# Kernel tuning notes

Measured on AMD Instinct MI355X. Metric: run time of the kernel, lower is better.

## Reference

```python
import jax, jax.numpy as jnp
import numpy as np

K_ORDER = 3
GRID_N = 10
GRID_LO, GRID_HI = -2.0, 2.0
LAYERS = [(49, 256), (256, 256), (256, 10)]
NCOEF = GRID_N + K_ORDER  # 13


def mish(x):
    return x * jnp.tanh(jax.nn.softplus(x))


def bspline_basis(x):
    # x: (B, in) -> basis (B, in, GRID_N + K_ORDER)
    h = (GRID_HI - GRID_LO) / GRID_N
    knots = GRID_LO + h * jnp.arange(-K_ORDER, GRID_N + K_ORDER + 1, dtype=x.dtype)  # (G+2k+1,)
    xx = x[..., None]
    B = ((xx >= knots[:-1]) & (xx < knots[1:])).astype(x.dtype)  # degree-0, (B,in,G+2k)
    for d in range(1, K_ORDER + 1):
        left = (xx - knots[: -(d + 1)]) / (knots[d:-1] - knots[: -(d + 1)]) * B[..., :-1]
        right = (knots[d + 1:] - xx) / (knots[d + 1:] - knots[1:-d]) * B[..., 1:]
        B = left + right
    return B  # (B, in, G+k)


def kan_layer(x, coef, scale_base, scale_sp, bias):
    # x: (B,in); coef: (in,out,G+k); scales: (in,out); bias: (out,)
    basis = bspline_basis(x)                                   # (B,in,G+k)
    spline = jnp.einsum('big,iog->bo', basis, coef * scale_sp[..., None])
    base = jnp.einsum('bi,io->bo', mish(x), scale_base)
    return base + spline + bias


def setup_inputs() -> dict:
    key = jax.random.key(0)
    ks = jax.random.split(key, 1 + 4 * len(LAYERS))
    inp = {'x': jax.random.normal(ks[0], (8192, 1, 28, 28), dtype=jnp.float32)}
    i = 1
    for li, (fin, fout) in enumerate(LAYERS, start=1):
        inp[f'coef{li}'] = 0.1 * jax.random.normal(ks[i], (fin, fout, NCOEF), dtype=jnp.float32); i += 1
        inp[f'sb{li}'] = 1.0 + 0.1 * jax.random.normal(ks[i], (fin, fout), dtype=jnp.float32); i += 1
        inp[f'sp{li}'] = 1.0 + 0.1 * jax.random.normal(ks[i], (fin, fout), dtype=jnp.float32); i += 1
        inp[f'b{li}'] = jnp.zeros((fout,), dtype=jnp.float32); i += 1
    return inp


def reference(x, coef1, sb1, sp1, b1, coef2, sb2, sp2, b2, coef3, sb3, sp3, b3):
    B = x.shape[0]
    # avg_pool2d(x, 4): 28x28 -> 7x7
    h = x.reshape(B, 1, 7, 4, 7, 4).mean(axis=(3, 5))
    h = h.reshape(B, 49)
    h = kan_layer(h, coef1, sb1, sp1, b1)
    h = kan_layer(h, coef2, sb2, sp2, b2)
    h = kan_layer(h, coef3, sb3, sp3, b3)
    return jax.nn.log_softmax(h, axis=1)
```

## Files before the change

kernel.cpp:

```cpp
#include <hip/hip_runtime.h>
#include <hip/hip_bf16.h>

typedef __bf16 bf16x8_t __attribute__((ext_vector_type(8)));
typedef float f32x4_t __attribute__((ext_vector_type(4)));
using bf16 = __hip_bfloat16;

#define ASG __attribute__((address_space(1)))
#define ASL __attribute__((address_space(3)))

__device__ __forceinline__ void gld_lds16(const void* g, void* l) {
  __builtin_amdgcn_global_load_lds((ASG void*)const_cast<void*>(g),
                                   (ASL void*)l, 16, 0, 0);
}

__device__ __forceinline__ unsigned short f2bf_bits(float v) {
  __hip_bfloat16 h = __float2bfloat16(v);
  return *reinterpret_cast<unsigned short*>(&h);
}

__device__ __forceinline__ float mish_f(float x) {
  float z = __expf(x);
  float n = z * (z + 2.0f);
  float m = x * n / (n + 2.0f);
  return (x > 10.0f) ? x : m;
}

__device__ __forceinline__ void kan_feats28(bf16* dst, float x) {
  unsigned int* d32 = (unsigned int*)dst;
#pragma unroll
  for (int d = 0; d < 7; ++d) d32[d] = 0u;
  float t = (x + 3.2f) * 2.5f;
  if (t >= 0.0f && t < 16.0f) {
    float tf = floorf(t);
    int c = (int)tf;
    float u = t - tf;
    float um = 1.0f - u;
    float u2 = u * u, u3 = u2 * u;
    const float s6 = 1.0f / 6.0f;
    float w0 = um * um * um * s6;
    float w1 = (3.0f * u3 - 6.0f * u2 + 4.0f) * s6;
    float w2 = (-3.0f * u3 + 3.0f * u2 + 3.0f * u + 1.0f) * s6;
    float w3 = u3 * s6;
    int j0 = c - 3;
    if (j0 >= 0)               dst[j0]     = __float2bfloat16(w0);
    if (j0 >= -1 && j0 <= 11)  dst[j0 + 1] = __float2bfloat16(w1);
    if (j0 >= -2 && j0 <= 10)  dst[j0 + 2] = __float2bfloat16(w2);
    if (j0 <= 9)               dst[j0 + 3] = __float2bfloat16(w3);
  }
  dst[13] = __float2bfloat16(mish_f(x));
}

__global__ __launch_bounds__(256) void prep_all(
    const float* __restrict__ c1, const float* __restrict__ sb1, const float* __restrict__ sp1,
    const float* __restrict__ c2, const float* __restrict__ sb2, const float* __restrict__ sp2,
    const float* __restrict__ c3, const float* __restrict__ sb3, const float* __restrict__ sp3,
    bf16* __restrict__ W1t, bf16* __restrict__ W2f, bf16* __restrict__ W3f) {
  const int b = blockIdx.x, o = threadIdx.x;
  float vals[14];
  if (b < 49) {
    const int i = b;
    const size_t io = (size_t)i * 256 + o;
    const float spv = sp1[io];
#pragma unroll
    for (int r = 0; r < 13; ++r) vals[r] = c1[io * 13 + r] * spv;
    vals[13] = sb1[io];
    unsigned int* dst = (unsigned int*)(W1t + (size_t)o * 704 + i * 14);
#pragma unroll
    for (int d = 0; d < 7; ++d)
      dst[d] = (unsigned int)f2bf_bits(vals[2 * d]) |
               ((unsigned int)f2bf_bits(vals[2 * d + 1]) << 16);
  } else if (b == 49) {
    unsigned int* dst = (unsigned int*)(W1t + (size_t)o * 704 + 686);
#pragma unroll
    for (int d = 0; d < 9; ++d) dst[d] = 0u;
  } else if (b < 306) {
    const int i = b - 50;
    const size_t io = (size_t)i * 256 + o;
    const float spv = sp2[io];
#pragma unroll
    for (int r = 0; r < 13; ++r) vals[r] = c2[io * 13 + r] * spv;
    vals[13] = sb2[io];
    const int ntg = o >> 4, lr = o & 15;
#pragma unroll
    for (int d = 0; d < 7; ++d) {
      const int k2 = i * 14 + 2 * d;
      const int kc = k2 / 224, rem = k2 % 224;
      const int ks = rem / 32, r2 = rem % 32, quad = r2 / 8, el = r2 % 8;
      const size_t off = ((size_t)((kc * 7 + ks) * 16 + ntg)) * 512 + lr * 32 + quad * 8 + el;
      *(unsigned int*)(W2f + off) = (unsigned int)f2bf_bits(vals[2 * d]) |
                                    ((unsigned int)f2bf_bits(vals[2 * d + 1]) << 16);
    }
  } else {
    const int i = b - 306;
    if (o < 10) {
      const size_t io = (size_t)i * 10 + o;
      const float spv = sp3[io];
#pragma unroll
      for (int r = 0; r < 13; ++r) vals[r] = c3[io * 13 + r] * spv;
      vals[13] = sb3[io];
#pragma unroll
      for (int d = 0; d < 7; ++d) {
        const int k2 = i * 14 + 2 * d;
        const int s = k2 >> 5, r2 = k2 & 31;
        const size_t off = (size_t)s * 512 + o * 32 + (r2 >> 3) * 8 + (r2 & 7);
        *(unsigned int*)(W3f + off) = (unsigned int)f2bf_bits(vals[2 * d]) |
                                      ((unsigned int)f2bf_bits(vals[2 * d + 1]) << 16);
      }
    } else if (o < 16) {
#pragma unroll
      for (int d = 0; d < 7; ++d) {
        const int k2 = i * 14 + 2 * d;
        const int s = k2 >> 5, r2 = k2 & 31;
        *(unsigned int*)(W3f + (size_t)s * 512 + o * 32 + (r2 >> 3) * 8 + (r2 & 7)) = 0u;
      }
    }
  }
}

__global__ __launch_bounds__(256) void pool_basis1(const float* __restrict__ x,
                                                   bf16* __restrict__ A1) {
  __shared__ __align__(16) float xs[3136];
  __shared__ __align__(16) bf16 arow[4 * 704];
  const int b4 = blockIdx.x * 4, t = threadIdx.x;
  const float4* xsrc = (const float4*)(x + (size_t)b4 * 784);
  float4* xd = (float4*)xs;
#pragma unroll
  for (int l = t; l < 784; l += 256) xd[l] = xsrc[l];
  __syncthreads();
  if (t < 196) {
    const int img = t / 49, p = t - img * 49;
    const int oh = p / 7, ow = p - oh * 7;
    const float* xi = xs + img * 784;
    float s = 0.f;
#pragma unroll
    for (int r = 0; r < 4; ++r)
#pragma unroll
      for (int c = 0; c < 4; ++c) s += xi[(oh * 4 + r) * 28 + ow * 4 + c];
    kan_feats28(&arow[img * 704 + p * 14], s * (1.0f / 16.0f));
  } else if (t < 232) {
    const int q = t - 196;
    const int img = q / 9, d = q - img * 9;
    ((unsigned int*)(arow + img * 704 + 686))[d] = 0u;
  }
  __syncthreads();
  uint4* dst = (uint4*)(A1 + (size_t)b4 * 704);
  const uint4* src = (const uint4*)arow;
#pragma unroll
  for (int l = t; l < 352; l += 256) dst[l] = src[l];
}

__global__ __launch_bounds__(256) void gemm1s(
    const bf16* __restrict__ A, const bf16* __restrict__ Wt,
    const float* __restrict__ bias, float* __restrict__ H) {
  constexpr int K = 704;
  __shared__ __align__(16) bf16 As[64 * 64];
  __shared__ __align__(16) bf16 Bs[64 * 64];
  const int t = threadIdx.x;
  const int wv = t >> 6, lane = t & 63, quad = lane >> 4, lr = lane & 15;
  const int n0 = blockIdx.x * 64;
  const int m0 = blockIdx.y * 64;
  const int srow0 = lane >> 3;
  const int cg = (lane & 7) ^ srow0;
  const bf16* gA0 = A + (size_t)(m0 + 8 * wv + srow0) * K + cg * 8;
  const bf16* gA1 = A + (size_t)(m0 + 32 + 8 * wv + srow0) * K + cg * 8;
  const bf16* gB0 = Wt + (size_t)(n0 + 8 * wv + srow0) * K + cg * 8;
  const bf16* gB1 = Wt + (size_t)(n0 + 32 + 8 * wv + srow0) * K + cg * 8;
  char* const lA = (char*)As + wv * 1024;
  char* const lB = (char*)Bs + wv * 1024;
  const int wm = (wv & 1) * 32, wn = (wv >> 1) * 32;
  const int swz = lr & 7;
  f32x4_t acc00 = {0.f, 0.f, 0.f, 0.f}, acc01 = acc00, acc10 = acc00, acc11 = acc00;
  for (int k0 = 0; k0 < K; k0 += 64) {
    gld_lds16(gA0 + k0, lA);
    gld_lds16(gA1 + k0, lA + 4096);
    gld_lds16(gB0 + k0, lB);
    gld_lds16(gB1 + k0, lB + 4096);
    __syncthreads();
#pragma unroll
    for (int s = 0; s < 2; ++s) {
      const int co = ((s * 4 + quad) ^ swz) * 16;
      bf16x8_t a0 = *(const bf16x8_t*)((char*)As + (wm + lr) * 128 + co);
      bf16x8_t a1 = *(const bf16x8_t*)((char*)As + (wm + 16 + lr) * 128 + co);
      bf16x8_t b0 = *(const bf16x8_t*)((char*)Bs + (wn + lr) * 128 + co);
      bf16x8_t b1 = *(const bf16x8_t*)((char*)Bs + (wn + 16 + lr) * 128 + co);
      acc00 = __builtin_amdgcn_mfma_f32_16x16x32_bf16(a0, b0, acc00, 0, 0, 0);
      acc01 = __builtin_amdgcn_mfma_f32_16x16x32_bf16(a0, b1, acc01, 0, 0, 0);
      acc10 = __builtin_amdgcn_mfma_f32_16x16x32_bf16(a1, b0, acc10, 0, 0, 0);
      acc11 = __builtin_amdgcn_mfma_f32_16x16x32_bf16(a1, b1, acc11, 0, 0, 0);
    }
    __syncthreads();
  }
  const int cb = n0 + wn + lr;
  const float bn0 = bias[cb], bn1 = bias[cb + 16];
#pragma unroll
  for (int r = 0; r < 4; ++r) {
    const size_t row = (size_t)(m0 + wm + quad * 4 + r);
    H[row * 256 + cb] = acc00[r] + bn0;
    H[row * 256 + cb + 16] = acc01[r] + bn1;
    H[(row + 16) * 256 + cb] = acc10[r] + bn0;
    H[(row + 16) * 256 + cb + 16] = acc11[r] + bn1;
  }
}

__global__ __launch_bounds__(512, 4) void kan_gemm2(
    const float* __restrict__ Hin, const bf16* __restrict__ W2f,
    float* __restrict__ Hp) {
  __shared__ __align__(16) bf16 As[2][64 * 232];
  const int t = threadIdx.x;
  const int w = t >> 6, lane = t & 63, quad = lane >> 4, lr = lane & 15;
  const int m0 = blockIdx.x * 64;
  const int z = blockIdx.y;
  const int ej = t & 15, er0 = (t >> 4) & 31;
  const int foff = lr * 32 + quad * 8;
  f32x4_t acc[4][2];
#pragma unroll
  for (int m = 0; m < 4; ++m) {
    acc[m][0] = (f32x4_t){0.f, 0.f, 0.f, 0.f};
    acc[m][1] = (f32x4_t){0.f, 0.f, 0.f, 0.f};
  }
  const float* hp = Hin + (size_t)(m0 + er0) * 256 + z * 64 + ej;
  kan_feats28(As[0] + er0 * 232 + ej * 14, hp[0]);
  kan_feats28(As[0] + (er0 + 32) * 232 + ej * 14, hp[32 * 256]);
  const bf16* wbase = W2f + ((size_t)(z * 28 * 16 + w * 2)) * 512 + foff;
  bf16x8_t p0[4], p1[4];
#pragma unroll
  for (int s = 0; s < 4; ++s) {
    p0[s] = *(const bf16x8_t*)(wbase + (size_t)s * 8192);
    p1[s] = *(const bf16x8_t*)(wbase + (size_t)s * 8192 + 512);
  }
#pragma unroll
  for (int kcl = 0; kcl < 4; ++kcl) {
    __syncthreads();
    const bf16* cur = As[kcl & 1];
    bf16* nxt = As[(kcl & 1) ^ 1];
#pragma unroll
    for (int ks = 0; ks < 7; ++ks) {
      const int step = kcl * 7 + ks;
      const int slot = step & 3;
      bf16x8_t b0 = p0[slot], b1 = p1[slot];
      if (step + 4 < 28) {
        p0[slot] = *(const bf16x8_t*)(wbase + (size_t)(step + 4) * 8192);
        p1[slot] = *(const bf16x8_t*)(wbase + (size_t)(step + 4) * 8192 + 512);
      }
#pragma unroll
      for (int m = 0; m < 4; ++m) {
        bf16x8_t a = *(const bf16x8_t*)(cur + (m * 16 + lr) * 232 + ks * 32 + quad * 8);
        acc[m][0] = __builtin_amdgcn_mfma_f32_16x16x32_bf16(a, b0, acc[m][0], 0, 0, 0);
        acc[m][1] = __builtin_amdgcn_mfma_f32_16x16x32_bf16(a, b1, acc[m][1], 0, 0, 0);
      }
    }
    if (kcl < 3) {
      kan_feats28(nxt + er0 * 232 + ej * 14, hp[(kcl + 1) * 16]);
      kan_feats28(nxt + (er0 + 32) * 232 + ej * 14, hp[32 * 256 + (kcl + 1) * 16]);
    }
  }
  float* Hpz = Hp + (size_t)z * (8192 * 256);
  const int c0 = w * 32 + lr;
#pragma unroll
  for (int m = 0; m < 4; ++m)
#pragma unroll
    for (int r = 0; r < 4; ++r) {
      const size_t row = (size_t)(m0 + m * 16 + quad * 4 + r);
      Hpz[row * 256 + c0] = acc[m][0][r];
      Hpz[row * 256 + c0 + 16] = acc[m][1][r];
    }
}

__global__ __launch_bounds__(256) void kan_gemm3(
    const float* __restrict__ Hp, const float* __restrict__ b2,
    const bf16* __restrict__ W3f, float* __restrict__ part) {
  __shared__ __align__(16) bf16 As[64 * 232];
  const int t = threadIdx.x;
  const int wv = t >> 6, lane = t & 63, quad = lane >> 4, lr = lane & 15;
  const int m0 = blockIdx.x * 64;
  const int z = blockIdx.y;
  const int ej = t & 15, er0 = t >> 4;
  const int foff = lr * 32 + quad * 8;
  f32x4_t acc = {0.f, 0.f, 0.f, 0.f};
#pragma unroll
  for (int kcl = 0; kcl < 2; ++kcl) {
    const int kc = z * 2 + kcl;
    const float bc = b2[kc * 16 + ej];
    const float* hp = Hp + (size_t)(m0 + er0) * 256 + kc * 16 + ej;
    if (kcl) __syncthreads();
#pragma unroll
    for (int e = 0; e < 4; ++e) {
      const size_t idx = (size_t)e * 16 * 256;
      float h = hp[idx] + hp[idx + 2097152] + hp[idx + 4194304] + hp[idx + 6291456] + bc;
      kan_feats28(As + (er0 + 16 * e) * 232 + ej * 14, h);
    }
    __syncthreads();
#pragma unroll
    for (int ks = 0; ks < 7; ++ks) {
      bf16x8_t b = *(const bf16x8_t*)(W3f + (size_t)(kc * 7 + ks) * 512 + foff);
      bf16x8_t a = *(const bf16x8_t*)(As + (wv * 16 + lr) * 232 + ks * 32 + quad * 8);
      acc = __builtin_amdgcn_mfma_f32_16x16x32_bf16(a, b, acc, 0, 0, 0);
    }
  }
#pragma unroll
  for (int r = 0; r < 4; ++r)
    part[(size_t)z * 131072 + (size_t)lr * 8192 + (m0 + wv * 16 + quad * 4 + r)] = acc[r];
}

__global__ __launch_bounds__(256) void lsm(const float* __restrict__ part,
                                           const float* __restrict__ b3,
                                           float* __restrict__ out) {
  const int row = blockIdx.x * 256 + threadIdx.x;
  float v[10];
#pragma unroll
  for (int o = 0; o < 10; ++o) {
    float s = b3[o];
#pragma unroll
    for (int kc = 0; kc < 8; ++kc) s += part[(size_t)kc * 131072 + (size_t)o * 8192 + row];
    v[o] = s;
  }
  float m = v[0];
#pragma unroll
  for (int o = 1; o < 10; ++o) m = fmaxf(m, v[o]);
  float se = 0.f;
#pragma unroll
  for (int o = 0; o < 10; ++o) se += expf(v[o] - m);
  const float l = m + logf(se);
#pragma unroll
  for (int o = 0; o < 10; ++o) out[(size_t)row * 10 + o] = v[o] - l;
}

extern "C" void kernel_launch(void* const* d_in, const int* in_sizes, int n_in,
                              void* d_out, int out_size, void* d_ws, size_t ws_size,
                              hipStream_t stream) {
  const float* x = (const float*)d_in[0];
  const float* coef1 = (const float*)d_in[1];
  const float* sb1 = (const float*)d_in[2];
  const float* sp1 = (const float*)d_in[3];
  const float* b1 = (const float*)d_in[4];
  const float* coef2 = (const float*)d_in[5];
  const float* sb2 = (const float*)d_in[6];
  const float* sp2 = (const float*)d_in[7];
  const float* b2 = (const float*)d_in[8];
  const float* coef3 = (const float*)d_in[9];
  const float* sb3 = (const float*)d_in[10];
  const float* sp3 = (const float*)d_in[11];
  const float* b3 = (const float*)d_in[12];
  float* out = (float*)d_out;

  char* ws = (char*)d_ws;
  size_t off = 0;
  bf16* A1 = (bf16*)(ws + off);    off += 11534336;
  bf16* W1t = (bf16*)(ws + off);   off += 360448;
  bf16* W2f = (bf16*)(ws + off);   off += 1835008;
  bf16* W3f = (bf16*)(ws + off);   off += 114688;
  float* H1 = (float*)(ws + off);  off += 8388608;
  float* Hp = (float*)(ws + off);  off += 33554432;
  float* part = (float*)(ws + off); off += 4194304;

  prep_all<<<562, 256, 0, stream>>>(coef1, sb1, sp1, coef2, sb2, sp2,
                                    coef3, sb3, sp3, W1t, W2f, W3f);
  pool_basis1<<<2048, 256, 0, stream>>>(x, A1);
  gemm1s<<<dim3(4, 128), 256, 0, stream>>>(A1, W1t, b1, H1);
  kan_gemm2<<<dim3(128, 4), 512, 0, stream>>>(H1, W2f, Hp);
  kan_gemm3<<<dim3(128, 8), 256, 0, stream>>>(Hp, b2, W3f, part);
  lsm<<<32, 256, 0, stream>>>(part, b3, out);
}
```

Before: 146.4 us.

## Merge weight prep with pooling kernel and single-buffer gemm2 for occupancy

Folds the pooling/basis kernel and the weight-prep kernel into one launch, with blocks split by index, to remove one kernel launch. In kan_gemm2 the double-buffered LDS tile becomes a single buffer, the weight prefetch depth drops from 4 to 3 stages, and launch bounds ask for 6 blocks per CU. kan_gemm3 gets launch bounds of 8 blocks. The trade is lost overlap of basis computation with MFMA work and an extra barrier per chunk, in return for less LDS and fewer registers so more waves can be resident.

```diff
diff --git a/kernel.cpp b/kernel.cpp
--- a/kernel.cpp
+++ b/kernel.cpp
@@ -50,12 +50,45 @@
   dst[13] = __float2bfloat16(mish_f(x));
 }
 
-__global__ __launch_bounds__(256) void prep_all(
+__global__ __launch_bounds__(256) void prep_pool(
+    const float* __restrict__ x,
     const float* __restrict__ c1, const float* __restrict__ sb1, const float* __restrict__ sp1,
     const float* __restrict__ c2, const float* __restrict__ sb2, const float* __restrict__ sp2,
     const float* __restrict__ c3, const float* __restrict__ sb3, const float* __restrict__ sp3,
-    bf16* __restrict__ W1t, bf16* __restrict__ W2f, bf16* __restrict__ W3f) {
-  const int b = blockIdx.x, o = threadIdx.x;
+    bf16* __restrict__ A1, bf16* __restrict__ W1t, bf16* __restrict__ W2f,
+    bf16* __restrict__ W3f) {
+  if (blockIdx.x < 2048) {
+    __shared__ __align__(16) float xs[3136];
+    __shared__ __align__(16) bf16 arow[4 * 704];
+    const int b4 = blockIdx.x * 4, t = threadIdx.x;
+    const float4* xsrc = (const float4*)(x + (size_t)b4 * 784);
+    float4* xd = (float4*)xs;
+#pragma unroll
+    for (int l = t; l < 784; l += 256) xd[l] = xsrc[l];
+    __syncthreads();
+    if (t < 196) {
+      const int img = t / 49, p = t - img * 49;
+      const int oh = p / 7, ow = p - oh * 7;
+      const float* xi = xs + img * 784;
+      float s = 0.f;
+#pragma unroll
+      for (int r = 0; r < 4; ++r)
+#pragma unroll
+        for (int c = 0; c < 4; ++c) s += xi[(oh * 4 + r) * 28 + ow * 4 + c];
+      kan_feats28(&arow[img * 704 + p * 14], s * (1.0f / 16.0f));
+    } else if (t < 232) {
+      const int q = t - 196;
+      const int img = q / 9, d = q - img * 9;
+      ((unsigned int*)(arow + img * 704 + 686))[d] = 0u;
+    }
+    __syncthreads();
+    uint4* dst = (uint4*)(A1 + (size_t)b4 * 704);
+    const uint4* src = (const uint4*)arow;
+#pragma unroll
+    for (int l = t; l < 352; l += 256) dst[l] = src[l];
+    return;
+  }
+  const int b = blockIdx.x - 2048, o = threadIdx.x;
   float vals[14];
   if (b < 49) {
     const int i = b;
@@ -115,38 +148,6 @@
       }
     }
   }
-}
-
-__global__ __launch_bounds__(256) void pool_basis1(const float* __restrict__ x,
-                                                   bf16* __restrict__ A1) {
-  __shared__ __align__(16) float xs[3136];
-  __shared__ __align__(16) bf16 arow[4 * 704];
-  const int b4 = blockIdx.x * 4, t = threadIdx.x;
-  const float4* xsrc = (const float4*)(x + (size_t)b4 * 784);
-  float4* xd = (float4*)xs;
-#pragma unroll
-  for (int l = t; l < 784; l += 256) xd[l] = xsrc[l];
-  __syncthreads();
-  if (t < 196) {
-    const int img = t / 49, p = t - img * 49;
-    const int oh = p / 7, ow = p - oh * 7;
-    const float* xi = xs + img * 784;
-    float s = 0.f;
-#pragma unroll
-    for (int r = 0; r < 4; ++r)
-#pragma unroll
-      for (int c = 0; c < 4; ++c) s += xi[(oh * 4 + r) * 28 + ow * 4 + c];
-    kan_feats28(&arow[img * 704 + p * 14], s * (1.0f / 16.0f));
-  } else if (t < 232) {
-    const int q = t - 196;
-    const int img = q / 9, d = q - img * 9;
-    ((unsigned int*)(arow + img * 704 + 686))[d] = 0u;
-  }
-  __syncthreads();
-  uint4* dst = (uint4*)(A1 + (size_t)b4 * 704);
-  const uint4* src = (const uint4*)arow;
-#pragma unroll
-  for (int l = t; l < 352; l += 256) dst[l] = src[l];
 }
 
 __global__ __launch_bounds__(256) void gemm1s(
@@ -202,10 +203,10 @@
   }
 }
 
-__global__ __launch_bounds__(512, 4) void kan_gemm2(
+__global__ __launch_bounds__(512, 6) void kan_gemm2(
     const float* __restrict__ Hin, const bf16* __restrict__ W2f,
     float* __restrict__ Hp) {
-  __shared__ __align__(16) bf16 As[2][64 * 232];
+  __shared__ __align__(16) bf16 As[64 * 232];
   const int t = threadIdx.x;
   const int w = t >> 6, lane = t & 63, quad = lane >> 4, lr = lane & 15;
   const int m0 = blockIdx.x * 64;
@@ -219,40 +220,35 @@
     acc[m][1] = (f32x4_t){0.f, 0.f, 0.f, 0.f};
   }
   const float* hp = Hin + (size_t)(m0 + er0) * 256 + z * 64 + ej;
-  kan_feats28(As[0] + er0 * 232 + ej * 14, hp[0]);
-  kan_feats28(As[0] + (er0 + 32) * 232 + ej * 14, hp[32 * 256]);
   const bf16* wbase = W2f + ((size_t)(z * 28 * 16 + w * 2)) * 512 + foff;
-  bf16x8_t p0[4], p1[4];
-#pragma unroll
-  for (int s = 0; s < 4; ++s) {
+  bf16x8_t p0[3], p1[3];
+#pragma unroll
+  for (int s = 0; s < 3; ++s) {
     p0[s] = *(const bf16x8_t*)(wbase + (size_t)s * 8192);
     p1[s] = *(const bf16x8_t*)(wbase + (size_t)s * 8192 + 512);
   }
 #pragma unroll
   for (int kcl = 0; kcl < 4; ++kcl) {
-    __syncthreads();
-    const bf16* cur = As[kcl & 1];
-    bf16* nxt = As[(kcl & 1) ^ 1];
+    kan_feats28(As + er0 * 232 + ej * 14, hp[kcl * 16]);
+    kan_feats28(As + (er0 + 32) * 232 + ej * 14, hp[32 * 256 + kcl * 16]);
+    __syncthreads();
 #pragma unroll
     for (int ks = 0; ks < 7; ++ks) {
       const int step = kcl * 7 + ks;
-      const int slot = step & 3;
+      const int slot = step % 3;
       bf16x8_t b0 = p0[slot], b1 = p1[slot];
-      if (step + 4 < 28) {
-        p0[slot] = *(const bf16x8_t*)(wbase + (size_t)(step + 4) * 8192);
-        p1[slot] = *(const bf16x8_t*)(wbase + (size_t)(step + 4) * 8192 + 512);
+      if (step + 3 < 28) {
+        p0[slot] = *(const bf16x8_t*)(wbase + (size_t)(step + 3) * 8192);
+        p1[slot] = *(const bf16x8_t*)(wbase + (size_t)(step + 3) * 8192 + 512);
       }
 #pragma unroll
       for (int m = 0; m < 4; ++m) {
-        bf16x8_t a = *(const bf16x8_t*)(cur + (m * 16 + lr) * 232 + ks * 32 + quad * 8);
+        bf16x8_t a = *(const bf16x8_t*)(As + (m * 16 + lr) * 232 + ks * 32 + quad * 8);
         acc[m][0] = __builtin_amdgcn_mfma_f32_16x16x32_bf16(a, b0, acc[m][0], 0, 0, 0);
         acc[m][1] = __builtin_amdgcn_mfma_f32_16x16x32_bf16(a, b1, acc[m][1], 0, 0, 0);
       }
     }
-    if (kcl < 3) {
-      kan_feats28(nxt + er0 * 232 + ej * 14, hp[(kcl + 1) * 16]);
-      kan_feats28(nxt + (er0 + 32) * 232 + ej * 14, hp[32 * 256 + (kcl + 1) * 16]);
-    }
+    __syncthreads();
   }
   float* Hpz = Hp + (size_t)z * (8192 * 256);
   const int c0 = w * 32 + lr;
@@ -266,7 +262,7 @@
     }
 }
 
-__global__ __launch_bounds__(256) void kan_gemm3(
+__global__ __launch_bounds__(256, 8) void kan_gemm3(
     const float* __restrict__ Hp, const float* __restrict__ b2,
     const bf16* __restrict__ W3f, float* __restrict__ part) {
   __shared__ __align__(16) bf16 As[64 * 232];
@@ -353,9 +349,8 @@
   float* Hp = (float*)(ws + off);  off += 33554432;
   float* part = (float*)(ws + off); off += 4194304;
 
-  prep_all<<<562, 256, 0, stream>>>(coef1, sb1, sp1, coef2, sb2, sp2,
-                                    coef3, sb3, sp3, W1t, W2f, W3f);
-  pool_basis1<<<2048, 256, 0, stream>>>(x, A1);
+  prep_pool<<<2610, 256, 0, stream>>>(x, coef1, sb1, sp1, coef2, sb2, sp2,
+                                      coef3, sb3, sp3, A1, W1t, W2f, W3f);
   gemm1s<<<dim3(4, 128), 256, 0, stream>>>(A1, W1t, b1, H1);
   kan_gemm2<<<dim3(128, 4), 512, 0, stream>>>(H1, W2f, Hp);
   kan_gemm3<<<dim3(128, 8), 256, 0, stream>>>(Hp, b2, W3f, part);
```

Result: no change. 145.7 us (-0.5%).
